# Kernel tuning notes

Hardware: AMD Instinct MI355X
Metric: run time of the kernel (lower is better)

Reference implementation:

```python
import jax, jax.numpy as jnp
import numpy as np

B, T, V, E, H = 4, 2048, 50257, 1024, 16
D = E // H  # head dim = 64

def _ln(x, g, b, eps=1e-5):
    mu = jnp.mean(x, axis=-1, keepdims=True)
    var = jnp.var(x, axis=-1, keepdims=True)
    return (x - mu) * jax.lax.rsqrt(var + eps) * g + b

def setup_inputs() -> dict:
    key = jax.random.key(0)
    ks = jax.random.split(key, 20)
    s = 0.02
    return {
        "ids": jax.random.randint(ks[0], (B, T), 0, V),
        "wte": jax.random.normal(ks[1], (V, E), jnp.float32) * s,
        "wpe": jax.random.normal(ks[2], (T, E), jnp.float32) * s,
        "wq": jax.random.normal(ks[3], (H, E, D), jnp.float32) * s,
        "wk": jax.random.normal(ks[4], (H, E, D), jnp.float32) * s,
        "wv": jax.random.normal(ks[5], (H, E, D), jnp.float32) * s,
        "bq": jnp.zeros((H, D), jnp.float32),
        "bk": jnp.zeros((H, D), jnp.float32),
        "bv": jnp.zeros((H, D), jnp.float32),
        "wproj": jax.random.normal(ks[6], (E, E), jnp.float32) * s,
        "bproj": jnp.zeros((E,), jnp.float32),
        "ln1_g": jnp.ones((E,), jnp.float32),
        "ln1_b": jnp.zeros((E,), jnp.float32),
        "ln2_g": jnp.ones((E,), jnp.float32),
        "ln2_b": jnp.zeros((E,), jnp.float32),
        "w_fc": jax.random.normal(ks[7], (E, 4 * E), jnp.float32) * s,
        "b_fc": jnp.zeros((4 * E,), jnp.float32),
        "w_out": jax.random.normal(ks[8], (4 * E, E), jnp.float32) * s,
        "b_out": jnp.zeros((E,), jnp.float32),
    }

def reference(ids, wte, wpe, wq, wk, wv, bq, bk, bv, wproj, bproj,
              ln1_g, ln1_b, ln2_g, ln2_b, w_fc, b_fc, w_out, b_out):
    t = ids.shape[1]
    x = wte[ids] + wpe[:t]                      # [B,T,E]
    # --- attention (all heads batched; faithful per-head math) ---
    h = _ln(x, ln1_g, ln1_b)
    q = jnp.einsum('btc,hcd->bhtd', h, wq) + bq[None, :, None, :]
    k = jnp.einsum('btc,hcd->bhtd', h, wk) + bk[None, :, None, :]
    v = jnp.einsum('btc,hcd->bhtd', h, wv) + bv[None, :, None, :]
    scores = jnp.einsum('bhtd,bhsd->bhts', q, k) * (1.0 / np.sqrt(D))
    causal = jnp.tril(jnp.ones((t, t), bool))
    scores = jnp.where(causal, scores, -jnp.inf)
    attn = jax.nn.softmax(scores, axis=-1)      # dropout = identity (eval)
    o = jnp.einsum('bhts,bhsd->bhtd', attn, v)
    o = jnp.transpose(o, (0, 2, 1, 3)).reshape(x.shape[0], t, E)  # concat heads
    x = x + o @ wproj + bproj
    # --- MLP ---
    h2 = _ln(x, ln2_g, ln2_b)
    m = jax.nn.gelu(h2 @ w_fc + b_fc, approximate=False) @ w_out + b_out
    return x + m
```

## Files before the change

### kernel.cpp

```cpp
#include <hip/hip_runtime.h>
#include <math.h>

#define BB 4
#define TT 2048
#define EE 1024
#define HH 16
#define DD 64
#define MM (BB*TT)

typedef unsigned short u16;
typedef __bf16 bf16x8 __attribute__((ext_vector_type(8)));
typedef float  f32x4  __attribute__((ext_vector_type(4)));

__device__ inline float bf2f(u16 u){ union{unsigned int i; float f;} v; v.i=((unsigned int)u)<<16; return v.f; }
__device__ inline u16 f2bf(float f){ union{float f; unsigned int i;} v; v.f=f; return (u16)((v.i + 0x7fffu + ((v.i>>16)&1u))>>16); }
__device__ inline u16 f2bf_trunc(float f){ union{float f; unsigned int i;} v; v.f=f; return (u16)(v.i>>16); }

__device__ inline void gload_lds16(const void* g, void* l){
  __builtin_amdgcn_global_load_lds((__attribute__((address_space(1))) void*)g,
                                   (__attribute__((address_space(3))) void*)l, 16, 0, 0);
}

__global__ __launch_bounds__(256) void transpose_tile(
    const float* __restrict__ W, u16* __restrict__ WT, int N, int K)
{
    __shared__ float t[32][33];
    const int n0 = blockIdx.x*32, k0 = blockIdx.y*32;
    const int tx = threadIdx.x, ty = threadIdx.y;
    #pragma unroll
    for (int j=0;j<4;j++)
        t[ty + j*8][tx] = W[(size_t)(k0 + ty + j*8)*N + n0 + tx];
    __syncthreads();
    #pragma unroll
    for (int j=0;j<4;j++)
        WT[(size_t)(n0 + ty + j*8)*K + k0 + tx] = f2bf(t[tx][ty + j*8]);
}

__global__ __launch_bounds__(256) void transpose_v(
    const u16* __restrict__ V, u16* __restrict__ VT)
{
    __shared__ u16 t[32][34];
    const int bh = blockIdx.z;
    const int t0 = blockIdx.x*32;
    const int d0 = blockIdx.y*32;
    const int tx = threadIdx.x, ty = threadIdx.y;
    const u16* Vb = V + (size_t)bh*TT*DD;
    u16* VTb = VT + (size_t)bh*TT*DD;
    #pragma unroll
    for (int j=0;j<4;j++)
        t[ty+j*8][tx] = Vb[(size_t)(t0+ty+j*8)*DD + d0+tx];
    __syncthreads();
    #pragma unroll
    for (int j=0;j<4;j++)
        VTb[(size_t)(d0+ty+j*8)*TT + t0+tx] = t[tx][ty+j*8];
}

__global__ __launch_bounds__(256) void repack_qkv_tiled(
    const float* __restrict__ wq, const float* __restrict__ wk, const float* __restrict__ wv,
    u16* __restrict__ WT)
{
    __shared__ float t[32][33];
    const int z = blockIdx.z, which = z>>4, hh = z&15;
    const int d0 = blockIdx.x*32, c0 = blockIdx.y*32;
    const int tx = threadIdx.x, ty = threadIdx.y;
    const float* w = which==0 ? wq : (which==1 ? wk : wv);
    #pragma unroll
    for (int j=0;j<4;j++)
        t[ty + j*8][tx] = w[((size_t)hh*EE + c0 + ty + j*8)*DD + d0 + tx];
    __syncthreads();
    #pragma unroll
    for (int j=0;j<4;j++)
        WT[(size_t)(which*1024 + hh*64 + d0 + ty + j*8)*1024 + c0 + tx] = f2bf(t[tx][ty + j*8]);
}

__global__ __launch_bounds__(256) void copy_bias_qkv(
    const float* __restrict__ bq, const float* __restrict__ bk, const float* __restrict__ bv,
    float* __restrict__ bias)
{
    int i = blockIdx.x*256 + threadIdx.x;
    const float* b = i<1024 ? bq : (i<2048 ? bk : bv);
    bias[i] = b[i & 1023];
}

__global__ __launch_bounds__(256) void embed_ln1(
    const int* __restrict__ ids, const float* __restrict__ wte, const float* __restrict__ wpe,
    const float* __restrict__ g, const float* __restrict__ b,
    float* __restrict__ x_out, u16* __restrict__ h_out)
{
    const int token = blockIdx.x;
    const int t = token & (TT-1);
    const int id = ids[token];
    const int tid = threadIdx.x;
    float vals[4]; float s=0.f, s2=0.f;
    #pragma unroll
    for (int i=0;i<4;i++){
        int e = tid + i*256;
        float v = wte[(size_t)id*EE + e] + wpe[(size_t)t*EE + e];
        vals[i]=v; s+=v; s2+=v*v;
    }
    for (int off=32; off>=1; off>>=1){ s += __shfl_xor(s,off); s2 += __shfl_xor(s2,off); }
    __shared__ float red[8];
    int wave=tid>>6, lane=tid&63;
    if (lane==0){ red[wave]=s; red[4+wave]=s2; }
    __syncthreads();
    s = red[0]+red[1]+red[2]+red[3];
    s2 = red[4]+red[5]+red[6]+red[7];
    float mu = s*(1.f/EE);
    float var = s2*(1.f/EE) - mu*mu;
    float rstd = rsqrtf(var + 1e-5f);
    #pragma unroll
    for (int i=0;i<4;i++){
        int e = tid + i*256; float v = vals[i];
        x_out[(size_t)token*EE + e] = v;
        h_out[(size_t)token*EE + e] = f2bf((v-mu)*rstd*g[e] + b[e]);
    }
}

__global__ __launch_bounds__(256) void ln_fwd(
    const float* __restrict__ xin, const float* __restrict__ g, const float* __restrict__ b,
    u16* __restrict__ hout)
{
    const int token = blockIdx.x;
    const int tid = threadIdx.x;
    float vals[4]; float s=0.f, s2=0.f;
    #pragma unroll
    for (int i=0;i<4;i++){
        int e = tid + i*256;
        float v = xin[(size_t)token*EE + e];
        vals[i]=v; s+=v; s2+=v*v;
    }
    for (int off=32; off>=1; off>>=1){ s += __shfl_xor(s,off); s2 += __shfl_xor(s2,off); }
    __shared__ float red[8];
    int wave=tid>>6, lane=tid&63;
    if (lane==0){ red[wave]=s; red[4+wave]=s2; }
    __syncthreads();
    s = red[0]+red[1]+red[2]+red[3];
    s2 = red[4]+red[5]+red[6]+red[7];
    float mu = s*(1.f/EE);
    float var = s2*(1.f/EE) - mu*mu;
    float rstd = rsqrtf(var + 1e-5f);
    #pragma unroll
    for (int i=0;i<4;i++){
        int e = tid + i*256; float v = vals[i];
        hout[(size_t)token*EE + e] = f2bf((v-mu)*rstd*g[e] + b[e]);
    }
}

#define VMCNTW(N) asm volatile("s_waitcnt vmcnt(" #N ")" ::: "memory")
#define LGKMW(N)  asm volatile("s_waitcnt lgkmcnt(" #N ")" ::: "memory")
#define SCHEDB()  __builtin_amdgcn_sched_barrier(0)
#define BAR()     { SCHEDB(); __builtin_amdgcn_s_barrier(); SCHEDB(); }

__device__ __forceinline__ bf16x8 fld(const u16* base, int row, int j){
    return *(const bf16x8*)&base[(row<<6) + ((j ^ (row&7))<<3)];
}

template<int MODE>
__global__ __launch_bounds__(512,2) void gemm256(
    const u16* __restrict__ A, const u16* __restrict__ BT, const float* __restrict__ bias,
    float* CoutF, const float* resid, u16* __restrict__ CoutH,
    u16* __restrict__ q_out, u16* __restrict__ k_out, u16* __restrict__ v_out,
    int Ndim, int Kdim)
{
    __shared__ alignas(16) u16 As[2][256*64];
    __shared__ alignas(16) u16 Bs[2][256*64];
    const int tid = threadIdx.x, wave = tid>>6, lane = tid&63;
    const int quad = (lane>>4)&3, l16 = lane&15;
    const int wr = wave>>2, wc = wave&3;

    const int nwg = gridDim.x;
    const int chunk = nwg>>3;
    int id = blockIdx.x;
    id = (id&7)*chunk + (id>>3);
    const int m0 = (id & 31) << 8;
    const int n0 = (id >> 5) << 8;

    const int rS = tid>>3;
    const int jS = (tid&7) ^ (rS&7);
    const size_t off0   = (size_t)rS*Kdim + (size_t)(jS<<3);
    const size_t ofs64K = (size_t)64*Kdim;
    const u16* pA = A  + (size_t)m0*Kdim;
    const u16* pB = BT + (size_t)n0*Kdim;

#define STAGE(ARR, GP, BUF, H, KT)                                             \
  { const u16* _g = (GP) + (size_t)((H)*128)*Kdim + (size_t)(KT)*64 + off0;    \
    gload_lds16(_g,          &ARR[BUF][(H)*8192 + wave*512]);                  \
    gload_lds16(_g + ofs64K, &ARR[BUF][(H)*8192 + 4096 + wave*512]); }

    STAGE(As, pA, 0, 0, 0);
    STAGE(Bs, pB, 0, 0, 0);
    STAGE(Bs, pB, 0, 1, 0);
    STAGE(As, pA, 0, 1, 0);
    STAGE(As, pA, 1, 0, 1);
    STAGE(Bs, pB, 1, 0, 1);
    STAGE(Bs, pB, 1, 1, 1);

    f32x4 acc[8][4];
    const f32x4 zf = {0.f,0.f,0.f,0.f};
    #pragma unroll
    for (int i=0;i<8;i++)
        #pragma unroll
        for (int j=0;j<4;j++) acc[i][j]=zf;

    bf16x8 af[4][2], bfr[4][2];

#define LDA(HROW)                                                              \
  { _Pragma("unroll") for (int mt=0; mt<4; mt++)                               \
    { _Pragma("unroll") for (int kh=0; kh<2; kh++)                             \
        af[mt][kh] = fld(Ab, (HROW) + (wr<<6) + (mt<<4) + l16, kh*4+quad); } }
#define LDB(HROW, NTB)                                                         \
  { _Pragma("unroll") for (int nt=0; nt<2; nt++)                               \
    { _Pragma("unroll") for (int kh=0; kh<2; kh++)                             \
        bfr[(NTB)+nt][kh] = fld(Bb, (HROW) + (wc<<5) + (nt<<4) + l16, kh*4+quad); } }
#define MFMA16(MT0, NT0)                                                       \
  __builtin_amdgcn_s_setprio(1);                                               \
  { _Pragma("unroll") for (int mt=0; mt<4; mt++)                               \
    { _Pragma("unroll") for (int nt=0; nt<2; nt++)                             \
      { _Pragma("unroll") for (int kh=0; kh<2; kh++)                           \
          acc[(MT0)+mt][(NT0)+nt] = __builtin_amdgcn_mfma_f32_16x16x32_bf16(   \
              af[mt][kh], bfr[(NT0)+nt][kh], acc[(MT0)+mt][(NT0)+nt], 0,0,0);  \
      } } }                                                                    \
  __builtin_amdgcn_s_setprio(0);

    VMCNTW(6);
    BAR();

    const int NT = Kdim>>6;
    for (int kt=0; kt<NT; ++kt){
        const int b = kt&1;
        const u16* Ab = As[b];
        const u16* Bb = Bs[b];
        LDA(0); LDB(0,0);
        if (kt+1 < NT) STAGE(As, pA, b^1, 1, kt+1);
        LGKMW(8);
        BAR(); LGKMW(0); SCHEDB();
        MFMA16(0,0);
        BAR();
        LDB(128,2);
        if (kt+2 < NT) STAGE(As, pA, b, 0, kt+2);
        BAR(); LGKMW(0); SCHEDB();
        MFMA16(0,2);
        BAR();
        LDA(128);
        if (kt+2 < NT) STAGE(Bs, pB, b, 0, kt+2);
        BAR(); LGKMW(0); SCHEDB();
        MFMA16(4,2);
        BAR();
        if (kt+2 < NT) STAGE(Bs, pB, b, 1, kt+2);
        BAR();
        MFMA16(4,0);
        if (kt+2 < NT)      { VMCNTW(6); }
        else if (kt+1 < NT) { VMCNTW(0); }
        BAR();
    }
#undef STAGE
#undef LDA
#undef LDB
#undef MFMA16

    #pragma unroll
    for (int mt=0; mt<8; mt++){
        const int mrow = m0 + ((mt<4) ? (wr<<6)+(mt<<4) : 128+(wr<<6)+((mt-4)<<4)) + (quad<<2);
        #pragma unroll
        for (int nt=0; nt<4; nt++){
            const int n = n0 + ((nt<2) ? (wc<<5)+(nt<<4) : 128+(wc<<5)+((nt-2)<<4)) + l16;
            #pragma unroll
            for (int r=0;r<4;r++){
                const int m = mrow + r;
                float v = acc[mt][nt][r] + bias[n];
                if (MODE==0){
                    int which = n>>10, hd = n&1023, hh = hd>>6, d = hd&63;
                    u16* dst = which==0 ? q_out : (which==1 ? k_out : v_out);
                    int bb = m>>11, t = m&(TT-1);
                    dst[(((size_t)(bb*HH+hh)*TT + t)<<6) + d] = f2bf(v);
                } else if (MODE==1){
                    size_t idx = (size_t)m*Ndim + n;
                    CoutF[idx] = resid[idx] + v;
                } else {
                    size_t idx = (size_t)m*Ndim + n;
                    CoutH[idx] = f2bf(0.5f*v*(1.0f + erff(v*0.70710678118f)));
                }
            }
        }
    }
}

template<int MODE>
__global__ __launch_bounds__(512,2) void gemm128(
    const u16* __restrict__ A, const u16* __restrict__ BT, const float* __restrict__ bias,
    float* CoutF, const float* resid, u16* __restrict__ CoutH,
    u16* __restrict__ q_out, u16* __restrict__ k_out, u16* __restrict__ v_out,
    int Ndim, int Kdim)
{
    __shared__ alignas(16) u16 As[2][128*64];
    __shared__ alignas(16) u16 Bs[2][256*64];
    const int tid = threadIdx.x, wave = tid>>6, lane = tid&63;
    const int quad = (lane>>4)&3, l16 = lane&15;
    const int wr = wave>>2, wc = wave&3;

    const int nwg = gridDim.x;
    const int chunk = nwg>>3;
    int id = blockIdx.x;
    id = (id&7)*chunk + (id>>3);
    const int nT = Ndim>>8;
    const int n0 = (id % nT) << 8;
    const int m0 = (id / nT) << 7;

    const int rS = tid>>3;
    const int jS = (tid&7) ^ (rS&7);
    const size_t off0 = (size_t)rS*Kdim + (size_t)(jS<<3);
    const u16* pA = A  + (size_t)m0*Kdim;
    const u16* pB = BT + (size_t)n0*Kdim;

#define STG(ARR, GP, BUF, U, KT)                                               \
    gload_lds16((GP) + (size_t)((U)*64)*Kdim + (size_t)(KT)*64 + off0,         \
                &ARR[BUF][(U)*4096 + wave*512]);

    STG(As,pA,0,0,0); STG(As,pA,0,1,0);
    STG(Bs,pB,0,0,0); STG(Bs,pB,0,1,0); STG(Bs,pB,0,2,0); STG(Bs,pB,0,3,0);
    STG(As,pA,1,0,1); STG(As,pA,1,1,1);
    STG(Bs,pB,1,0,1); STG(Bs,pB,1,1,1); STG(Bs,pB,1,2,1); STG(Bs,pB,1,3,1);

    f32x4 acc[4][4];
    const f32x4 zf = {0.f,0.f,0.f,0.f};
    #pragma unroll
    for (int i=0;i<4;i++)
        #pragma unroll
        for (int j=0;j<4;j++) acc[i][j]=zf;

    bf16x8 af[4][2], bfr[2][2];

#define LDA8()                                                                 \
  { _Pragma("unroll") for (int mt=0; mt<4; mt++)                               \
    { _Pragma("unroll") for (int kh=0; kh<2; kh++)                             \
        af[mt][kh] = fld(Ab, (wr<<6) + (mt<<4) + l16, kh*4+quad); } }
#define LDB4(NTB)                                                              \
  { _Pragma("unroll") for (int nt=0; nt<2; nt++)                               \
    { _Pragma("unroll") for (int kh=0; kh<2; kh++)                             \
        bfr[nt][kh] = fld(Bb, (wc<<6) + (((NTB)+nt)<<4) + l16, kh*4+quad); } }
#define MFMA16B(NT0)                                                           \
  __builtin_amdgcn_s_setprio(1);                                               \
  { _Pragma("unroll") for (int mt=0; mt<4; mt++)                               \
    { _Pragma("unroll") for (int nt=0; nt<2; nt++)                             \
      { _Pragma("unroll") for (int kh=0; kh<2; kh++)                           \
          acc[mt][(NT0)+nt] = __builtin_amdgcn_mfma_f32_16x16x32_bf16(         \
              af[mt][kh], bfr[nt][kh], acc[mt][(NT0)+nt], 0,0,0);              \
      } } }                                                                    \
  __builtin_amdgcn_s_setprio(0);

    VMCNTW(6);
    BAR();

    const int NT = Kdim>>6;
    for (int kt=0; kt<NT; ++kt){
        const int b = kt&1;
        const u16* Ab = As[b];
        const u16* Bb = Bs[b];
        LDA8(); LDB4(0);
        LGKMW(8);
        BAR(); LGKMW(0); SCHEDB();
        MFMA16B(0);
        BAR();
        LDB4(2);
        if (kt+2 < NT){
            STG(As,pA,b,0,kt+2); STG(As,pA,b,1,kt+2);
            STG(Bs,pB,b,0,kt+2); STG(Bs,pB,b,1,kt+2);
        }
        BAR(); LGKMW(0); SCHEDB();
        MFMA16B(2);
        BAR();
        if (kt+2 < NT){
            STG(Bs,pB,b,2,kt+2); STG(Bs,pB,b,3,kt+2);
            VMCNTW(6);
        } else if (kt+1 < NT) { VMCNTW(0); }
        BAR();
    }
#undef STG
#undef LDA8
#undef LDB4
#undef MFMA16B

    #pragma unroll
    for (int mt=0; mt<4; mt++){
        const int mrow = m0 + (wr<<6) + (mt<<4) + (quad<<2);
        #pragma unroll
        for (int nt=0; nt<4; nt++){
            const int n = n0 + (wc<<6) + (nt<<4) + l16;
            #pragma unroll
            for (int r=0;r<4;r++){
                const int m = mrow + r;
                float v = acc[mt][nt][r] + bias[n];
                if (MODE==0){
                    int which = n>>10, hd = n&1023, hh = hd>>6, d = hd&63;
                    u16* dst = which==0 ? q_out : (which==1 ? k_out : v_out);
                    int bb = m>>11, t = m&(TT-1);
                    dst[(((size_t)(bb*HH+hh)*TT + t)<<6) + d] = f2bf(v);
                } else if (MODE==1){
                    size_t idx = (size_t)m*Ndim + n;
                    CoutF[idx] = resid[idx] + v;
                } else {
                    size_t idx = (size_t)m*Ndim + n;
                    CoutH[idx] = f2bf(0.5f*v*(1.0f + erff(v*0.70710678118f)));
                }
            }
        }
    }
}

__device__ __forceinline__ void attn_proc_tile(
    int kt, int q0, int quad, int l16,
    const u16* Ks, const u16* Vs, u16* Psw,
    const bf16x8 (&qf)[2][2], f32x4 (&oacc)[2][4], float (&lsum)[2][4])
{
    if (kt > ((q0+31)>>6)) return;
    const f32x4 zf = {0.f,0.f,0.f,0.f};
    f32x4 a[2][4];
    #pragma unroll
    for (int m=0;m<2;m++)
        #pragma unroll
        for (int st=0;st<4;st++) a[m][st]=zf;
    #pragma unroll
    for (int h2=0;h2<2;h2++){
        #pragma unroll
        for (int st=0;st<4;st++){
            const int s = st*16 + l16;
            const int jc = h2*4 + quad;
            bf16x8 kf = *(const bf16x8*)&Ks[s*64 + (jc ^ (s&7))*8];
            #pragma unroll
            for (int m=0;m<2;m++)
                a[m][st] = __builtin_amdgcn_mfma_f32_16x16x32_bf16(qf[m][h2], kf, a[m][st], 0,0,0);
        }
    }
    const bool needMask = (kt*64 + 63 > q0);
    #pragma unroll
    for (int m=0;m<2;m++){
        const int q0m = q0 + m*16;
        #pragma unroll
        for (int st=0;st<4;st++){
            #pragma unroll
            for (int r=0;r<4;r++){
                float p = exp2f(fminf(a[m][st][r]*0.1803369f, 40.f));
                if (needMask){
                    const int qrow = q0m + quad*4 + r;
                    const int s = kt*64 + st*16 + l16;
                    if (s > qrow) p = 0.f;
                }
                lsum[m][r] += p;
                const int ql = m*16 + quad*4 + r;
                const int sc3 = st*2 + (l16>>3);
                Psw[ql*64 + (sc3 ^ (ql&7))*8 + (l16&7)] = f2bf_trunc(p);
            }
        }
    }
    #pragma unroll
    for (int kh=0; kh<2; kh++){
        const int jc = kh*4 + quad;
        bf16x8 pf[2];
        #pragma unroll
        for (int m=0;m<2;m++){
            const int ql16 = m*16 + l16;
            pf[m] = *(const bf16x8*)&Psw[ql16*64 + (jc ^ (ql16&7))*8];
        }
        #pragma unroll
        for (int dt=0; dt<4; dt++){
            const int d = dt*16 + l16;
            bf16x8 vf = *(const bf16x8*)&Vs[d*64 + (jc ^ (d&7))*8];
            #pragma unroll
            for (int m=0;m<2;m++)
                oacc[m][dt] = __builtin_amdgcn_mfma_f32_16x16x32_bf16(pf[m], vf, oacc[m][dt], 0,0,0);
        }
    }
}

__global__ __launch_bounds__(256,2) void attn_kernel(
    const u16* __restrict__ Q, const u16* __restrict__ K, const u16* __restrict__ VT,
    u16* __restrict__ O)
{
    __shared__ u16 Ks[64*64];
    __shared__ u16 Vs[64*64];
    __shared__ u16 Ps[4*2048];
    const int tid = threadIdx.x, wave = tid>>6, lane = tid&63;
    const int quad = lane>>4, l16 = lane&15;
    const int id = blockIdx.x;
    const int bh   = (id&7) | ((id>>6)<<3);
    const int pair = (id>>3)&7;
    const int qtA = pair, qtB = 15-pair;
    const size_t base = (size_t)bh*TT*DD;
    const u16* Qb = Q + base;
    const u16* Kb = K + base;
    const u16* VTb = VT + base;
    const int qA0 = qtA*128 + wave*32;
    const int qB0 = qtB*128 + wave*32;
    u16* Psw = &Ps[wave*2048];

    bf16x8 qfA[2][2], qfB[2][2];
    #pragma unroll
    for (int m=0;m<2;m++)
        #pragma unroll
        for (int h2=0;h2<2;h2++){
            qfA[m][h2] = *(const bf16x8*)&Qb[(size_t)(qA0+m*16+l16)*DD + h2*32 + quad*8];
            qfB[m][h2] = *(const bf16x8*)&Qb[(size_t)(qB0+m*16+l16)*DD + h2*32 + quad*8];
        }

    const f32x4 zf = {0.f,0.f,0.f,0.f};
    f32x4 oaccA[2][4], oaccB[2][4];
    float lsumA[2][4], lsumB[2][4];
    #pragma unroll
    for (int m=0;m<2;m++){
        #pragma unroll
        for (int dt=0;dt<4;dt++){ oaccA[m][dt]=zf; oaccB[m][dt]=zf; }
        #pragma unroll
        for (int r=0;r<4;r++){ lsumA[m][r]=0.f; lsumB[m][r]=0.f; }
    }

    const int ktMax = 31 - 2*pair;

    const int c0 = wave*64 + lane, c1 = 256 + wave*64 + lane;
    const int r0 = c0>>3, j0 = (c0&7) ^ (r0&7);
    const int r1 = c1>>3, j1 = (c1&7) ^ (r1&7);

    for (int kt=0; kt<=ktMax; kt++){
        __syncthreads();
        {
            const int s0 = kt*64;
            gload_lds16(Kb  + (size_t)(s0+r0)*DD + j0*8, &Ks[wave*512]);
            gload_lds16(Kb  + (size_t)(s0+r1)*DD + j1*8, &Ks[(4+wave)*512]);
            gload_lds16(VTb + (size_t)r0*TT + s0 + j0*8, &Vs[wave*512]);
            gload_lds16(VTb + (size_t)r1*TT + s0 + j1*8, &Vs[(4+wave)*512]);
        }
        __syncthreads();
        attn_proc_tile(kt, qB0, quad, l16, Ks, Vs, Psw, qfB, oaccB, lsumB);
        attn_proc_tile(kt, qA0, quad, l16, Ks, Vs, Psw, qfA, oaccA, lsumA);
    }

    #pragma unroll
    for (int off=1; off<16; off<<=1)
        #pragma unroll
        for (int m=0;m<2;m++)
            #pragma unroll
            for (int r=0;r<4;r++){
                lsumA[m][r] += __shfl_xor(lsumA[m][r], off);
                lsumB[m][r] += __shfl_xor(lsumB[m][r], off);
            }

    const int bb = bh>>4, hh = bh&15;
    #pragma unroll
    for (int m=0;m<2;m++)
        #pragma unroll
        for (int dt=0;dt<4;dt++)
            #pragma unroll
            for (int r=0;r<4;r++){
                int t = qA0 + m*16 + quad*4 + r;
                O[(size_t)(bb*TT + t)*EE + hh*64 + dt*16 + l16] = f2bf(oaccA[m][dt][r] / lsumA[m][r]);
                t = qB0 + m*16 + quad*4 + r;
                O[(size_t)(bb*TT + t)*EE + hh*64 + dt*16 + l16] = f2bf(oaccB[m][dt][r] / lsumB[m][r]);
            }
}

extern "C" void kernel_launch(void* const* d_in, const int* in_sizes, int n_in,
                              void* d_out, int out_size, void* d_ws, size_t ws_size,
                              hipStream_t stream)
{
    (void)in_sizes; (void)n_in; (void)out_size; (void)ws_size;
    const int*   ids  = (const int*)d_in[0];
    const float* wte  = (const float*)d_in[1];
    const float* wpe  = (const float*)d_in[2];
    const float* wq   = (const float*)d_in[3];
    const float* wk   = (const float*)d_in[4];
    const float* wv   = (const float*)d_in[5];
    const float* bq   = (const float*)d_in[6];
    const float* bk   = (const float*)d_in[7];
    const float* bv   = (const float*)d_in[8];
    const float* wproj= (const float*)d_in[9];
    const float* bproj= (const float*)d_in[10];
    const float* ln1g = (const float*)d_in[11];
    const float* ln1b = (const float*)d_in[12];
    const float* ln2g = (const float*)d_in[13];
    const float* ln2b = (const float*)d_in[14];
    const float* wfc  = (const float*)d_in[15];
    const float* bfc  = (const float*)d_in[16];
    const float* wout = (const float*)d_in[17];
    const float* bout = (const float*)d_in[18];

    const size_t MTOK = (size_t)MM*EE;
    char* p = (char*)d_ws;
    float* x    = (float*)p;  p += MTOK*sizeof(float);
    u16*  h     = (u16*)p;    p += MTOK*sizeof(u16);
    u16*  Qb    = (u16*)p;    p += MTOK*sizeof(u16);
    u16*  Kb    = (u16*)p;    p += MTOK*sizeof(u16);
    u16*  Vb    = (u16*)p;    p += MTOK*sizeof(u16);
    u16*  Ob    = (u16*)p;    p += MTOK*sizeof(u16);
    u16*  fcact = Qb;
    u16*  VTv   = h;
    u16*  WqkvT = (u16*)p;    p += (size_t)3072*1024*sizeof(u16);
    float* biasq= (float*)p;  p += 3072*sizeof(float);
    u16*  wprojT= (u16*)p;    p += (size_t)1024*1024*sizeof(u16);
    u16*  wfcT  = (u16*)p;    p += (size_t)4096*1024*sizeof(u16);
    u16*  woutT = (u16*)p;    p += (size_t)1024*4096*sizeof(u16);
    float* out  = (float*)d_out;

    repack_qkv_tiled<<<dim3(2,32,48),dim3(32,8),0,stream>>>(wq,wk,wv,WqkvT);
    copy_bias_qkv<<<12,256,0,stream>>>(bq,bk,bv,biasq);
    transpose_tile<<<dim3(32,32), dim3(32,8),0,stream>>>(wproj, wprojT, 1024, 1024);
    transpose_tile<<<dim3(128,32),dim3(32,8),0,stream>>>(wfc,   wfcT,   4096, 1024);
    transpose_tile<<<dim3(32,128),dim3(32,8),0,stream>>>(wout,  woutT,  1024, 4096);
    embed_ln1<<<MM,256,0,stream>>>(ids, wte, wpe, ln1g, ln1b, x, h);
    gemm128<0><<<768,512,0,stream>>>(h, WqkvT, biasq, nullptr,nullptr,nullptr, Qb,Kb,Vb, 3072, 1024);
    transpose_v<<<dim3(64,2,64),dim3(32,8),0,stream>>>(Vb, VTv);
    attn_kernel<<<512,256,0,stream>>>(Qb,Kb,VTv,Ob);
    gemm128<1><<<256,512,0,stream>>>(Ob, wprojT, bproj, x, x, nullptr, nullptr,nullptr,nullptr, 1024, 1024);
    ln_fwd<<<MM,256,0,stream>>>(x, ln2g, ln2b, h);
    gemm256<2><<<512,512,0,stream>>>(h, wfcT, bfc, nullptr,nullptr, fcact, nullptr,nullptr,nullptr, 4096, 1024);
    gemm128<1><<<256,512,0,stream>>>(fcact, woutT, bout, out, x, nullptr, nullptr,nullptr,nullptr, 1024, 4096);
}
```

Measured before the change: 742.7 us.

## Double-buffer attention K/V tiles, add MFMA priority hints, specialize GEMM kernels

The attention kernel now keeps two K/V tile buffers in shared memory and prefetches the next tile with async global-to-LDS loads while the current tile is processed. This replaces the two full barriers around a synchronous load. MFMA sections get s_setprio raised so the wave scheduler favours matrix work. The GEMMs are wrapped in per-shape kernels with compile-time N/K dimensions, which could let the compiler fold the constants. The extra LDS buffer may lower occupancy.

```diff
diff --git a/kernel.cpp b/kernel.cpp
--- a/kernel.cpp
+++ b/kernel.cpp
@@ -156,7 +156,27 @@
 }
 
 template<int MODE>
-__global__ __launch_bounds__(512,2) void gemm256(
+__device__ __forceinline__ void epi_write(
+    int m, int n, float v, int Ndim,
+    float* CoutF, const float* resid, u16* CoutH,
+    u16* q_out, u16* k_out, u16* v_out)
+{
+    if (MODE==0){
+        int which = n>>10, hd = n&1023, hh = hd>>6, d = hd&63;
+        u16* dst = which==0 ? q_out : (which==1 ? k_out : v_out);
+        int bb = m>>11, t = m&(TT-1);
+        dst[(((size_t)(bb*HH+hh)*TT + t)<<6) + d] = f2bf(v);
+    } else if (MODE==1){
+        size_t idx = (size_t)m*Ndim + n;
+        CoutF[idx] = resid[idx] + v;
+    } else {
+        size_t idx = (size_t)m*Ndim + n;
+        CoutH[idx] = f2bf(0.5f*v*(1.0f + erff(v*0.70710678118f)));
+    }
+}
+
+template<int MODE>
+__device__ __forceinline__ void gemm256_body(
     const u16* __restrict__ A, const u16* __restrict__ BT, const float* __restrict__ bias,
     float* CoutF, const float* resid, u16* __restrict__ CoutH,
     u16* __restrict__ q_out, u16* __restrict__ k_out, u16* __restrict__ v_out,
@@ -265,28 +285,15 @@
         for (int nt=0; nt<4; nt++){
             const int n = n0 + ((nt<2) ? (wc<<5)+(nt<<4) : 128+(wc<<5)+((nt-2)<<4)) + l16;
             #pragma unroll
-            for (int r=0;r<4;r++){
-                const int m = mrow + r;
-                float v = acc[mt][nt][r] + bias[n];
-                if (MODE==0){
-                    int which = n>>10, hd = n&1023, hh = hd>>6, d = hd&63;
-                    u16* dst = which==0 ? q_out : (which==1 ? k_out : v_out);
-                    int bb = m>>11, t = m&(TT-1);
-                    dst[(((size_t)(bb*HH+hh)*TT + t)<<6) + d] = f2bf(v);
-                } else if (MODE==1){
-                    size_t idx = (size_t)m*Ndim + n;
-                    CoutF[idx] = resid[idx] + v;
-                } else {
-                    size_t idx = (size_t)m*Ndim + n;
-                    CoutH[idx] = f2bf(0.5f*v*(1.0f + erff(v*0.70710678118f)));
-                }
-            }
+            for (int r=0;r<4;r++)
+                epi_write<MODE>(mrow + r, n, acc[mt][nt][r] + bias[n], Ndim,
+                                CoutF, resid, CoutH, q_out, k_out, v_out);
         }
     }
 }
 
 template<int MODE>
-__global__ __launch_bounds__(512,2) void gemm128(
+__device__ __forceinline__ void gemm128_body(
     const u16* __restrict__ A, const u16* __restrict__ BT, const float* __restrict__ bias,
     float* CoutF, const float* resid, u16* __restrict__ CoutH,
     u16* __restrict__ q_out, u16* __restrict__ k_out, u16* __restrict__ v_out,
@@ -387,24 +394,36 @@
         for (int nt=0; nt<4; nt++){
             const int n = n0 + (wc<<6) + (nt<<4) + l16;
             #pragma unroll
-            for (int r=0;r<4;r++){
-                const int m = mrow + r;
-                float v = acc[mt][nt][r] + bias[n];
-                if (MODE==0){
-                    int which = n>>10, hd = n&1023, hh = hd>>6, d = hd&63;
-                    u16* dst = which==0 ? q_out : (which==1 ? k_out : v_out);
-                    int bb = m>>11, t = m&(TT-1);
-                    dst[(((size_t)(bb*HH+hh)*TT + t)<<6) + d] = f2bf(v);
-                } else if (MODE==1){
-                    size_t idx = (size_t)m*Ndim + n;
-                    CoutF[idx] = resid[idx] + v;
-                } else {
-                    size_t idx = (size_t)m*Ndim + n;
-                    CoutH[idx] = f2bf(0.5f*v*(1.0f + erff(v*0.70710678118f)));
-                }
-            }
-        }
-    }
+            for (int r=0;r<4;r++)
+                epi_write<MODE>(mrow + r, n, acc[mt][nt][r] + bias[n], Ndim,
+                                CoutF, resid, CoutH, q_out, k_out, v_out);
+        }
+    }
+}
+
+__global__ __launch_bounds__(512,2) void gemm_qkv(
+    const u16* __restrict__ A, const u16* __restrict__ BT, const float* __restrict__ bias,
+    u16* __restrict__ q_out, u16* __restrict__ k_out, u16* __restrict__ v_out)
+{
+    gemm128_body<0>(A, BT, bias, nullptr, nullptr, nullptr, q_out, k_out, v_out, 3072, 1024);
+}
+__global__ __launch_bounds__(512,2) void gemm_proj(
+    const u16* __restrict__ A, const u16* __restrict__ BT, const float* __restrict__ bias,
+    float* CoutF, const float* resid)
+{
+    gemm128_body<1>(A, BT, bias, CoutF, resid, nullptr, nullptr, nullptr, nullptr, 1024, 1024);
+}
+__global__ __launch_bounds__(512,2) void gemm_out(
+    const u16* __restrict__ A, const u16* __restrict__ BT, const float* __restrict__ bias,
+    float* CoutF, const float* resid)
+{
+    gemm128_body<1>(A, BT, bias, CoutF, resid, nullptr, nullptr, nullptr, nullptr, 1024, 4096);
+}
+__global__ __launch_bounds__(512,2) void gemm_fc(
+    const u16* __restrict__ A, const u16* __restrict__ BT, const float* __restrict__ bias,
+    u16* __restrict__ CoutH)
+{
+    gemm256_body<2>(A, BT, bias, nullptr, nullptr, CoutH, nullptr, nullptr, nullptr, 4096, 1024);
 }
 
 __device__ __forceinline__ void attn_proc_tile(
@@ -419,6 +438,7 @@
     for (int m=0;m<2;m++)
         #pragma unroll
         for (int st=0;st<4;st++) a[m][st]=zf;
+    __builtin_amdgcn_s_setprio(1);
     #pragma unroll
     for (int h2=0;h2<2;h2++){
         #pragma unroll
@@ -431,6 +451,7 @@
                 a[m][st] = __builtin_amdgcn_mfma_f32_16x16x32_bf16(qf[m][h2], kf, a[m][st], 0,0,0);
         }
     }
+    __builtin_amdgcn_s_setprio(0);
     const bool needMask = (kt*64 + 63 > q0);
     #pragma unroll
     for (int m=0;m<2;m++){
@@ -452,6 +473,7 @@
             }
         }
     }
+    __builtin_amdgcn_s_setprio(1);
     #pragma unroll
     for (int kh=0; kh<2; kh++){
         const int jc = kh*4 + quad;
@@ -470,14 +492,15 @@
                 oacc[m][dt] = __builtin_amdgcn_mfma_f32_16x16x32_bf16(pf[m], vf, oacc[m][dt], 0,0,0);
         }
     }
+    __builtin_amdgcn_s_setprio(0);
 }
 
 __global__ __launch_bounds__(256,2) void attn_kernel(
     const u16* __restrict__ Q, const u16* __restrict__ K, const u16* __restrict__ VT,
     u16* __restrict__ O)
 {
-    __shared__ u16 Ks[64*64];
-    __shared__ u16 Vs[64*64];
+    __shared__ u16 Ks[2][64*64];
+    __shared__ u16 Vs[2][64*64];
     __shared__ u16 Ps[4*2048];
     const int tid = threadIdx.x, wave = tid>>6, lane = tid&63;
     const int quad = lane>>4, l16 = lane&15;
@@ -501,6 +524,7 @@
             qfA[m][h2] = *(const bf16x8*)&Qb[(size_t)(qA0+m*16+l16)*DD + h2*32 + quad*8];
             qfB[m][h2] = *(const bf16x8*)&Qb[(size_t)(qB0+m*16+l16)*DD + h2*32 + quad*8];
         }
+    VMCNTW(0); SCHEDB();
 
     const f32x4 zf = {0.f,0.f,0.f,0.f};
     f32x4 oaccA[2][4], oaccB[2][4];
@@ -519,19 +543,24 @@
     const int r0 = c0>>3, j0 = (c0&7) ^ (r0&7);
     const int r1 = c1>>3, j1 = (c1&7) ^ (r1&7);
 
+#define STAGEKV(KT, BUF)                                                       \
+  { const int s0 = (KT)*64;                                                    \
+    gload_lds16(Kb  + (size_t)(s0+r0)*DD + j0*8, &Ks[BUF][wave*512]);          \
+    gload_lds16(Kb  + (size_t)(s0+r1)*DD + j1*8, &Ks[BUF][(4+wave)*512]);      \
+    gload_lds16(VTb + (size_t)r0*TT + s0 + j0*8, &Vs[BUF][wave*512]);          \
+    gload_lds16(VTb + (size_t)r1*TT + s0 + j1*8, &Vs[BUF][(4+wave)*512]); }
+
+    STAGEKV(0, 0);
     for (int kt=0; kt<=ktMax; kt++){
-        __syncthreads();
-        {
-            const int s0 = kt*64;
-            gload_lds16(Kb  + (size_t)(s0+r0)*DD + j0*8, &Ks[wave*512]);
-            gload_lds16(Kb  + (size_t)(s0+r1)*DD + j1*8, &Ks[(4+wave)*512]);
-            gload_lds16(VTb + (size_t)r0*TT + s0 + j0*8, &Vs[wave*512]);
-            gload_lds16(VTb + (size_t)r1*TT + s0 + j1*8, &Vs[(4+wave)*512]);
-        }
-        __syncthreads();
-        attn_proc_tile(kt, qB0, quad, l16, Ks, Vs, Psw, qfB, oaccB, lsumB);
-        attn_proc_tile(kt, qA0, quad, l16, Ks, Vs, Psw, qfA, oaccA, lsumA);
-    }
+        const int b = kt&1;
+        if (kt < ktMax){ STAGEKV(kt+1, b^1); VMCNTW(4); }
+        else           { VMCNTW(0); }
+        BAR();
+        attn_proc_tile(kt, qB0, quad, l16, Ks[b], Vs[b], Psw, qfB, oaccB, lsumB);
+        attn_proc_tile(kt, qA0, quad, l16, Ks[b], Vs[b], Psw, qfA, oaccA, lsumA);
+        BAR();
+    }
+#undef STAGEKV
 
     #pragma unroll
     for (int off=1; off<16; off<<=1)
@@ -605,11 +634,11 @@
     transpose_tile<<<dim3(128,32),dim3(32,8),0,stream>>>(wfc,   wfcT,   4096, 1024);
     transpose_tile<<<dim3(32,128),dim3(32,8),0,stream>>>(wout,  woutT,  1024, 4096);
     embed_ln1<<<MM,256,0,stream>>>(ids, wte, wpe, ln1g, ln1b, x, h);
-    gemm128<0><<<768,512,0,stream>>>(h, WqkvT, biasq, nullptr,nullptr,nullptr, Qb,Kb,Vb, 3072, 1024);
+    gemm_qkv<<<768,512,0,stream>>>(h, WqkvT, biasq, Qb, Kb, Vb);
     transpose_v<<<dim3(64,2,64),dim3(32,8),0,stream>>>(Vb, VTv);
     attn_kernel<<<512,256,0,stream>>>(Qb,Kb,VTv,Ob);
-    gemm128<1><<<256,512,0,stream>>>(Ob, wprojT, bproj, x, x, nullptr, nullptr,nullptr,nullptr, 1024, 1024);
+    gemm_proj<<<256,512,0,stream>>>(Ob, wprojT, bproj, x, x);
     ln_fwd<<<MM,256,0,stream>>>(x, ln2g, ln2b, h);
-    gemm256<2><<<512,512,0,stream>>>(h, wfcT, bfc, nullptr,nullptr, fcact, nullptr,nullptr,nullptr, 4096, 1024);
-    gemm128<1><<<256,512,0,stream>>>(fcact, woutT, bout, out, x, nullptr, nullptr,nullptr,nullptr, 1024, 4096);
-}
+    gemm_fc<<<512,512,0,stream>>>(h, wfcT, bfc, fcact);
+    gemm_out<<<256,512,0,stream>>>(fcact, woutT, bout, out, x);
+}
```

New measurement: 740.5 us. Within noise of the previous version (-0.3%).
